# Kernel tuning notes

Measured on AMD Instinct MI355X. Metric: run time of the kernel, lower is better.

Reference implementation:

```python
import jax, jax.numpy as jnp
import numpy as np

OBS_DIM = 128
ACT_DIM = 32
N_AGENTS = 16   # == max_agents; all agents active (obs[...,0]==1)
BATCH = 48
HID = 128       # hid_dim (state encoder output / actor hidden)
QHID = 128      # q_hid_dim (RSA embed dim inside Q)
HEADS = 4       # nn.MultiheadAttention default heads used by Q's RSABlock


def _lin(key, out_d, in_d):
    """torch nn.Linear default init: U(-1/sqrt(fan_in), 1/sqrt(fan_in))."""
    kw, kb = jax.random.split(key)
    s = 1.0 / np.sqrt(in_d)
    w = jax.random.uniform(kw, (out_d, in_d), minval=-s, maxval=s, dtype=jnp.float32)
    b = jax.random.uniform(kb, (out_d,), minval=-s, maxval=s, dtype=jnp.float32)
    return w, b


def linear(x, w, b):
    return x @ w.T + b


def setup_inputs() -> dict:
    key = jax.random.key(0)
    ks = jax.random.split(key, 12)
    obs = jax.random.normal(ks[0], (BATCH, N_AGENTS, OBS_DIM), dtype=jnp.float32)
    obs = obs.at[:, :, 0].set(1.0)  # every agent active
    aw1, ab1 = _lin(ks[1], 2 * HID, OBS_DIM)          # Actor.hidden_layer1
    aw2, ab2 = _lin(ks[2], HID, 2 * HID)              # Actor.hidden_layer2
    aw3, ab3 = _lin(ks[3], ACT_DIM, HID)              # Actor.action_layer
    eow, eob = _lin(ks[4], HID, OBS_DIM)              # StateEncoder.obs_encode_layer
    eaw, eab = _lin(ks[5], HID, OBS_DIM + ACT_DIM)    # StateEncoder.obs_act_encode_layer
    riw, rib = _lin(ks[6], QHID, HID)                 # Q RSABlock.input_layer
    row, rob = _lin(ks[7], QHID, QHID)                # Q RSABlock.output_layer
    miw, mib = _lin(ks[8], 3 * QHID, QHID)            # MHA in_proj
    mow, mob = _lin(ks[9], QHID, QHID)                # MHA out_proj
    qw, qb = _lin(ks[10], 1, QHID)                    # Q.q_layer
    return dict(obs=obs, aw1=aw1, ab1=ab1, aw2=aw2, ab2=ab2, aw3=aw3, ab3=ab3,
                eow=eow, eob=eob, eaw=eaw, eab=eab, riw=riw, rib=rib,
                row=row, rob=rob, miw=miw, mib=mib, mow=mow, mob=mob,
                qw=qw, qb=qb)


def reference(obs, aw1, ab1, aw2, ab2, aw3, ab3, eow, eob, eaw, eab,
              riw, rib, row, rob, miw, mib, mow, mob, qw, qb):
    B, N, _ = obs.shape
    # ---- Actor (all agents active -> fully batched) ----
    x = jax.nn.leaky_relu(linear(obs, aw1, ab1))
    x = jax.nn.leaky_relu(linear(x, aw2, ab2))
    logits = jax.nn.gelu(linear(x, aw3, ab3), approximate=False)  # torch exact GELU
    policy = logits  # (B, N, A)
    # ---- StateEncoder ----
    eo = linear(obs, eow, eob)                                   # (B, N, HID)
    ea = linear(jnp.concatenate([obs, policy], -1), eaw, eab)    # (B, N, HID)
    # counterfactual for agent i: [encoded_obs_i, encoded_obs_act_{j != i}]
    idx = np.array([[j for j in range(N) if j != i] for i in range(N)])  # (N, N-1)
    cf = jnp.concatenate([eo[:, :, None, :], ea[:, idx, :]], axis=2)     # (B, N, N, HID)
    # ---- Q (RSABlock; MHA is batch_first=False -> seq dim = B*N!) ----
    L = B * N
    x1 = jax.nn.relu(linear(cf.reshape(L, N, HID), riw, rib))    # (L, N, E)
    hd = QHID // HEADS
    q, k, v = jnp.split(linear(x1, miw, mib), 3, axis=-1)
    sh = (L, N, HEADS, hd)
    scores = jnp.einsum('lbhd,mbhd->bhlm', q.reshape(sh), k.reshape(sh)) / np.sqrt(hd)
    attn = jax.nn.softmax(scores, axis=-1)                       # (N, H, L, L)
    ao = jnp.einsum('bhlm,mbhd->lbhd', attn, v.reshape(sh)).reshape(L, N, QHID)
    ao = linear(ao, mow, mob)
    ctx = jax.nn.relu(linear(ao + x1, row, rob))                 # (L, N, E)
    qv = linear(ctx, qw, qb).reshape(B, N, N, 1)
    q_values = jnp.sum(qv, axis=2)                               # (B, N, 1)
    policy_flat = policy.reshape(B, N * ACT_DIM)
    return (policy_flat, q_values, eo)
```

## Files before the change

kernel.cpp:

```cpp
#include <hip/hip_runtime.h>
#include <math.h>

static __device__ __forceinline__ float lrelu(float x){ return x > 0.f ? x : 0.01f * x; }

#define OFF_XE    196608
#define OFF_XA    294912
#define OFF_QKVE  393216
#define OFF_QKVA  688128
#define OFF_AOP   983040
#define OFF_DEN   1376256
#define OFF_AOA   1388544
#define OFF_QVE   1572864
#define OFF_QVA   1573632
#define WS_FLOATS 1575072

#define OUT_POL 0
#define OUT_QV  24576
#define OUT_EO  25344

#define SCALE_ATTN 0.17677669529663689f

#define PHASE_FENCE() __builtin_amdgcn_sched_barrier(0)

template<int NCHUNK>
static __device__ __forceinline__ void phase_dot(
    const float* __restrict__ wbase,
    const float* __restrict__ x0, const float* __restrict__ x1,
    const float* __restrict__ x2, const float* __restrict__ x3,
    float* __restrict__ accs)
{
  #pragma unroll 1
  for (int ch = 0; ch < NCHUNK; ++ch) {
    const float4* wp = (const float4*)(wbase + ch * 32);
    float4 wf[8];
    #pragma unroll
    for (int i = 0; i < 8; ++i) wf[i] = wp[i];
    const float* xr0 = x0 + ch * 32;
    const float* xr1 = x1 + ch * 32;
    const float* xr2 = x2 + ch * 32;
    const float* xr3 = x3 + ch * 32;
    #pragma unroll
    for (int r = 0; r < 4; ++r) {
      const float* xr = (r == 0) ? xr0 : (r == 1) ? xr1 : (r == 2) ? xr2 : xr3;
      float ax = 0.f, ay = 0.f, az = 0.f, aw = 0.f;
      #pragma unroll
      for (int i = 0; i < 8; ++i) {
        float4 x = *(const float4*)&xr[i * 4];
        ax = fmaf(x.x, wf[i].x, ax); ay = fmaf(x.y, wf[i].y, ay);
        az = fmaf(x.z, wf[i].z, az); aw = fmaf(x.w, wf[i].w, aw);
      }
      accs[r] += (ax + ay) + (az + aw);
    }
  }
}

static __device__ __forceinline__ void tail_mac2(const float4* __restrict__ wp,
    const float* __restrict__ x0, const float* __restrict__ x1,
    const float* __restrict__ x2, const float* __restrict__ x3,
    float* __restrict__ accs)
{
  float4 wf[2];
  #pragma unroll
  for (int i = 0; i < 2; ++i) wf[i] = wp[i];
  #pragma unroll
  for (int r = 0; r < 4; ++r) {
    const float* xr = (r == 0) ? x0 : (r == 1) ? x1 : (r == 2) ? x2 : x3;
    float ax = 0.f, ay = 0.f, az = 0.f, aw = 0.f;
    #pragma unroll
    for (int i = 0; i < 2; ++i) {
      float4 x = *(const float4*)&xr[i * 4];
      ax = fmaf(x.x, wf[i].x, ax); ay = fmaf(x.y, wf[i].y, ay);
      az = fmaf(x.z, wf[i].z, az); aw = fmaf(x.w, wf[i].w, aw);
    }
    accs[r] += (ax + ay) + (az + aw);
  }
}

__global__ __launch_bounds__(512, 1) void k12ws_front(
    const float* __restrict__ obs,
    const float* __restrict__ aw1, const float* __restrict__ ab1,
    const float* __restrict__ aw2, const float* __restrict__ ab2,
    const float* __restrict__ aw3, const float* __restrict__ ab3,
    const float* __restrict__ eow, const float* __restrict__ eob,
    const float* __restrict__ eaw, const float* __restrict__ eab,
    const float* __restrict__ riw, const float* __restrict__ rib,
    const float* __restrict__ miw, const float* __restrict__ mib,
    float* __restrict__ out, float* __restrict__ ws)
{
  __shared__ float sA[4][256];
  __shared__ float sB[4][160];
  __shared__ float sC[4][128];
  const int t  = threadIdx.x;
  const int bx = blockIdx.x;
  const bool isE = (bx < 192);
  const int r0 = (isE ? bx : bx - 192) * 4;

  const int c = (t & 15) | ((t >> 6) << 4);
  const int h = (t >> 4) & 3;
  const bool h0 = (t & 48) == 0;

  {
    int ri = t >> 7, k = t & 127;
    sB[ri][k] = obs[(r0 + ri) * 128 + k];
  }
  __syncthreads();
  PHASE_FENCE();

  if (isE) {
    {
      float accs[4] = {0.f, 0.f, 0.f, 0.f};
      phase_dot<1>(eow + c * 128 + h * 32,
                   &sB[0][h*32], &sB[1][h*32], &sB[2][h*32], &sB[3][h*32], accs);
      const float bias = eob[c];
      #pragma unroll
      for (int r = 0; r < 4; ++r) {
        float acc = accs[r];
        acc += __shfl_xor(acc, 16);
        acc += __shfl_xor(acc, 32);
        if (h0) {
          float v = acc + bias;
          sA[r][c] = v;
          out[OUT_EO + (r0 + r) * 128 + c] = v;
        }
      }
    }
    __syncthreads();
    PHASE_FENCE();
    {
      float accs[4] = {0.f, 0.f, 0.f, 0.f};
      phase_dot<1>(riw + c * 128 + h * 32,
                   &sA[0][h*32], &sA[1][h*32], &sA[2][h*32], &sA[3][h*32], accs);
      const float bias = rib[c];
      #pragma unroll
      for (int r = 0; r < 4; ++r) {
        float acc = accs[r];
        acc += __shfl_xor(acc, 16);
        acc += __shfl_xor(acc, 32);
        if (h0) {
          float v = fmaxf(acc + bias, 0.f);
          sC[r][c] = v;
          ws[OFF_XE + (r0 + r) * 128 + c] = v;
        }
      }
    }
    __syncthreads();
    PHASE_FENCE();
    #pragma unroll 1
    for (int g = 0; g < 3; ++g) {
      float accs[4] = {0.f, 0.f, 0.f, 0.f};
      phase_dot<1>(miw + (size_t)(g * 128 + c) * 128 + h * 32,
                   &sC[0][h*32], &sC[1][h*32], &sC[2][h*32], &sC[3][h*32], accs);
      const float bias = mib[g * 128 + c];
      #pragma unroll
      for (int r = 0; r < 4; ++r) {
        float acc = accs[r];
        acc += __shfl_xor(acc, 16);
        acc += __shfl_xor(acc, 32);
        if (h0)
          ws[OFF_QKVE + (size_t)(r0 + r) * 384 + g * 128 + c] = acc + bias;
      }
    }
  } else {
    #pragma unroll 1
    for (int g = 0; g < 2; ++g) {
      float accs[4] = {0.f, 0.f, 0.f, 0.f};
      phase_dot<1>(aw1 + (size_t)(g * 128 + c) * 128 + h * 32,
                   &sB[0][h*32], &sB[1][h*32], &sB[2][h*32], &sB[3][h*32], accs);
      const float bias = ab1[g * 128 + c];
      #pragma unroll
      for (int r = 0; r < 4; ++r) {
        float acc = accs[r];
        acc += __shfl_xor(acc, 16);
        acc += __shfl_xor(acc, 32);
        if (h0) sA[r][g * 128 + c] = lrelu(acc + bias);
      }
    }
    __syncthreads();
    PHASE_FENCE();
    {
      float accs[4] = {0.f, 0.f, 0.f, 0.f};
      phase_dot<2>(aw2 + (size_t)c * 256 + h * 64,
                   &sA[0][h*64], &sA[1][h*64], &sA[2][h*64], &sA[3][h*64], accs);
      const float bias = ab2[c];
      #pragma unroll
      for (int r = 0; r < 4; ++r) {
        float acc = accs[r];
        acc += __shfl_xor(acc, 16);
        acc += __shfl_xor(acc, 32);
        if (h0) sC[r][c] = lrelu(acc + bias);
      }
    }
    __syncthreads();
    PHASE_FENCE();
    if (t < 128) {
      const int c2 = (t & 15) | ((t >> 6) << 4);
      const int h2 = (t >> 4) & 3;
      float accs[4] = {0.f, 0.f, 0.f, 0.f};
      phase_dot<1>(aw3 + (size_t)c2 * 128 + h2 * 32,
                   &sC[0][h2*32], &sC[1][h2*32], &sC[2][h2*32], &sC[3][h2*32], accs);
      const float bias = ab3[c2];
      #pragma unroll
      for (int r = 0; r < 4; ++r) {
        float acc = accs[r];
        acc += __shfl_xor(acc, 16);
        acc += __shfl_xor(acc, 32);
        if ((t & 48) == 0) {
          float a = acc + bias;
          float g = 0.5f * a * (1.f + erff(a * 0.70710678118654752f));
          sB[r][128 + c2] = g;
          out[OUT_POL + (r0 + r) * 32 + c2] = g;
        }
      }
    }
    __syncthreads();
    PHASE_FENCE();
    {
      float accs[4] = {0.f, 0.f, 0.f, 0.f};
      const float* wb = eaw + (size_t)c * 160 + h * 40;
      phase_dot<1>(wb, &sB[0][h*40], &sB[1][h*40], &sB[2][h*40], &sB[3][h*40], accs);
      tail_mac2((const float4*)(wb + 32),
                &sB[0][h*40+32], &sB[1][h*40+32], &sB[2][h*40+32], &sB[3][h*40+32], accs);
      const float bias = eab[c];
      #pragma unroll
      for (int r = 0; r < 4; ++r) {
        float acc = accs[r];
        acc += __shfl_xor(acc, 16);
        acc += __shfl_xor(acc, 32);
        if (h0) sA[r][c] = acc + bias;
      }
    }
    __syncthreads();
    PHASE_FENCE();
    {
      float accs[4] = {0.f, 0.f, 0.f, 0.f};
      phase_dot<1>(riw + c * 128 + h * 32,
                   &sA[0][h*32], &sA[1][h*32], &sA[2][h*32], &sA[3][h*32], accs);
      const float bias = rib[c];
      #pragma unroll
      for (int r = 0; r < 4; ++r) {
        float acc = accs[r];
        acc += __shfl_xor(acc, 16);
        acc += __shfl_xor(acc, 32);
        if (h0) {
          float v = fmaxf(acc + bias, 0.f);
          sC[r][c] = v;
          ws[OFF_XA + (r0 + r) * 128 + c] = v;
        }
      }
    }
    __syncthreads();
    PHASE_FENCE();
    #pragma unroll 1
    for (int g = 0; g < 3; ++g) {
      float accs[4] = {0.f, 0.f, 0.f, 0.f};
      phase_dot<1>(miw + (size_t)(g * 128 + c) * 128 + h * 32,
                   &sC[0][h*32], &sC[1][h*32], &sC[2][h*32], &sC[3][h*32], accs);
      const float bias = mib[g * 128 + c];
      #pragma unroll
      for (int r = 0; r < 4; ++r) {
        float acc = accs[r];
        acc += __shfl_xor(acc, 16);
        acc += __shfl_xor(acc, 32);
        if (h0)
          ws[OFF_QKVA + (size_t)(r0 + r) * 384 + g * 128 + c] = acc + bias;
      }
    }
  }
}

__global__ __launch_bounds__(256) void k356_attn(float* __restrict__ ws)
{
  __shared__ __align__(16) union {
    struct { float Qs[16 * 36]; float KsT[32 * 68]; float VsT[32 * 68]; float Ss[16 * 68]; } e;
    struct { float Qb[48 * 33]; float Ka[96 * 33]; float Va[96 * 36]; float Ss[48 * 97]; float rinv[48]; } a;
  } su;
  const int t  = threadIdx.x;
  const int bx = blockIdx.x;

  if (bx < 768) {
    const int l0 = (bx % 48) * 16, h = (bx / 48) & 3, sp = bx / 192;
    const float* qkve = ws + OFF_QKVE;

    for (int f = t; f < 512; f += 256)
      su.e.Qs[(f >> 5) * 36 + (f & 31)] = qkve[(size_t)(l0 + (f >> 5)) * 384 + h * 32 + (f & 31)];
    __syncthreads();

    const int l = t >> 4, j = t & 15, c0 = j * 4;
    float q[32];
    #pragma unroll
    for (int dd = 0; dd < 8; ++dd) {
      float4 qq = *(const float4*)&su.e.Qs[l * 36 + dd * 4];
      q[dd*4+0] = qq.x; q[dd*4+1] = qq.y; q[dd*4+2] = qq.z; q[dd*4+3] = qq.w;
    }
    float o0 = 0.f, o1 = 0.f, dsum = 0.f;

    for (int mt = sp * 3; mt < sp * 3 + 3; ++mt) {
      const int m0 = mt * 64;
      __syncthreads();
      for (int f = t; f < 2048; f += 256) {
        int i = f >> 5, d = f & 31;
        const float* src = qkve + (size_t)(m0 + i) * 384 + h * 32 + d;
        su.e.KsT[d * 68 + i] = src[128];
        su.e.VsT[d * 68 + i] = src[256];
      }
      __syncthreads();

      float s0 = 0.f, s1 = 0.f, s2 = 0.f, s3 = 0.f;
      #pragma unroll
      for (int d = 0; d < 32; ++d) {
        float4 kk = *(const float4*)&su.e.KsT[d * 68 + c0];
        s0 = fmaf(q[d], kk.x, s0); s1 = fmaf(q[d], kk.y, s1);
        s2 = fmaf(q[d], kk.z, s2); s3 = fmaf(q[d], kk.w, s3);
      }
      s0 = expf(s0 * SCALE_ATTN); s1 = expf(s1 * SCALE_ATTN);
      s2 = expf(s2 * SCALE_ATTN); s3 = expf(s3 * SCALE_ATTN);
      float4 sv; sv.x = s0; sv.y = s1; sv.z = s2; sv.w = s3;
      *(float4*)&su.e.Ss[l * 68 + c0] = sv;
      float psum = (s0 + s1) + (s2 + s3);
      psum += __shfl_xor(psum, 1); psum += __shfl_xor(psum, 2);
      psum += __shfl_xor(psum, 4); psum += __shfl_xor(psum, 8);
      dsum += psum;

      float t0x=0.f,t0y=0.f,t0z=0.f,t0w=0.f, t1x=0.f,t1y=0.f,t1z=0.f,t1w=0.f;
      #pragma unroll
      for (int k4 = 0; k4 < 16; ++k4) {
        float4 p  = *(const float4*)&su.e.Ss[l * 68 + k4 * 4];
        float4 va = *(const float4*)&su.e.VsT[j * 68 + k4 * 4];
        float4 vb = *(const float4*)&su.e.VsT[(j + 16) * 68 + k4 * 4];
        t0x = fmaf(p.x, va.x, t0x); t0y = fmaf(p.y, va.y, t0y);
        t0z = fmaf(p.z, va.z, t0z); t0w = fmaf(p.w, va.w, t0w);
        t1x = fmaf(p.x, vb.x, t1x); t1y = fmaf(p.y, vb.y, t1y);
        t1z = fmaf(p.z, vb.z, t1z); t1w = fmaf(p.w, vb.w, t1w);
      }
      o0 += (t0x + t0y) + (t0z + t0w);
      o1 += (t1x + t1y) + (t1z + t1w);
    }

    float* aop = ws + OFF_AOP + (size_t)sp * 98304;
    aop[(size_t)(l0 + l) * 128 + h * 32 + j]      = o0;
    aop[(size_t)(l0 + l) * 128 + h * 32 + j + 16] = o1;
    if (j == 0) ws[OFF_DEN + sp * 3072 + (l0 + l) * 4 + h] = dsum;
  } else {
    const int z  = bx - 768;
    const int j1 = z >> 3;
    const int h  = (z & 7) >> 1, rb = z & 1;
    const int jj = j1 + 1;
    const float* qkva = ws + OFF_QKVA;

    for (int f = t; f < 3072; f += 256) {
      int ml = f >> 5, d = f & 31;
      int bp = ml >> 1, spar = ml & 1;
      int ag = spar ? jj : (jj - 1);
      const float* src = qkva + (size_t)(bp * 16 + ag) * 384 + h * 32 + d;
      su.a.Ka[ml * 33 + d] = src[128];
      su.a.Va[ml * 36 + d] = src[256];
    }
    for (int f = t; f < 1536; f += 256) {
      int ql = f >> 5, d = f & 31;
      int Lb = rb * 48 + ql;
      int b = Lb >> 1, s = Lb & 1;
      int ag = s ? jj : (jj - 1);
      su.a.Qb[ql * 33 + d] = qkva[(size_t)(b * 16 + ag) * 384 + h * 32 + d];
    }
    __syncthreads();

    {
      const int tl = (t >> 4) * 3, tm = (t & 15) * 6;
      float acc[3][6] = {{0.f}};
      #pragma unroll
      for (int d = 0; d < 32; ++d) {
        float qv[3], kv[6];
        #pragma unroll
        for (int r = 0; r < 3; ++r) qv[r] = su.a.Qb[(tl + r) * 33 + d];
        #pragma unroll
        for (int c = 0; c < 6; ++c) kv[c] = su.a.Ka[(tm + c) * 33 + d];
        #pragma unroll
        for (int r = 0; r < 3; ++r)
          #pragma unroll
          for (int c = 0; c < 6; ++c) acc[r][c] = fmaf(qv[r], kv[c], acc[r][c]);
      }
      const float wj = (float)jj, wnj = (float)(16 - jj);
      float rs[3] = {0.f, 0.f, 0.f};
      #pragma unroll
      for (int r = 0; r < 3; ++r)
        #pragma unroll
        for (int c = 0; c < 6; ++c) {
          float w = ((tm + c) & 1) ? wj : wnj;
          float p = w * expf(acc[r][c] * SCALE_ATTN);
          su.a.Ss[(tl + r) * 97 + tm + c] = p;
          rs[r] += p;
        }
      #pragma unroll
      for (int r = 0; r < 3; ++r) {
        rs[r] += __shfl_xor(rs[r], 1); rs[r] += __shfl_xor(rs[r], 2);
        rs[r] += __shfl_xor(rs[r], 4); rs[r] += __shfl_xor(rs[r], 8);
      }
      if ((t & 15) == 0) {
        su.a.rinv[tl + 0] = 1.f / rs[0];
        su.a.rinv[tl + 1] = 1.f / rs[1];
        su.a.rinv[tl + 2] = 1.f / rs[2];
      }
    }
    __syncthreads();

    if (t < 192) {
      const int l0 = (t >> 3) * 2, d0 = (t & 7) * 4;
      float a0x=0.f,a0y=0.f,a0z=0.f,a0w=0.f, a1x=0.f,a1y=0.f,a1z=0.f,a1w=0.f;
      for (int m = 0; m < 96; ++m) {
        float p0 = su.a.Ss[l0 * 97 + m], p1 = su.a.Ss[(l0 + 1) * 97 + m];
        float4 v = *(const float4*)&su.a.Va[m * 36 + d0];
        a0x = fmaf(p0, v.x, a0x); a0y = fmaf(p0, v.y, a0y);
        a0z = fmaf(p0, v.z, a0z); a0w = fmaf(p0, v.w, a0w);
        a1x = fmaf(p1, v.x, a1x); a1y = fmaf(p1, v.y, a1y);
        a1z = fmaf(p1, v.z, a1z); a1w = fmaf(p1, v.w, a1w);
      }
      const float s0 = su.a.rinv[l0], s1 = su.a.rinv[l0 + 1];
      float* ao = ws + OFF_AOA + (size_t)(j1 * 96 + rb * 48 + l0) * 128 + h * 32 + d0;
      float4 o0; o0.x = a0x * s0; o0.y = a0y * s0; o0.z = a0z * s0; o0.w = a0w * s0;
      float4 o1; o1.x = a1x * s1; o1.y = a1y * s1; o1.z = a1z * s1; o1.w = a1w * s1;
      *(float4*)ao = o0;
      *(float4*)(ao + 128) = o1;
    }
  }
}

__global__ __launch_bounds__(512, 1) void k7ab_epi(
    const float* __restrict__ mow, const float* __restrict__ mob,
    const float* __restrict__ roww, const float* __restrict__ robb,
    const float* __restrict__ qw,  const float* __restrict__ qb,
    float* __restrict__ ws)
{
  __shared__ float rows_in[8][132];
  __shared__ float res[8][132];
  __shared__ float t1s[8][132];
  __shared__ float qpart[8][8];
  const int t  = threadIdx.x;
  const int r0 = blockIdx.x * 8;

  for (int s = t; s < 1024; s += 512) {
    int ri = s >> 7, c = s & 127;
    int r = r0 + ri;
    float aoval, x1v;
    if (r < 768) {
      float num = ws[OFF_AOP + 0*98304 + (size_t)r*128 + c]
                + ws[OFF_AOP + 1*98304 + (size_t)r*128 + c]
                + ws[OFF_AOP + 2*98304 + (size_t)r*128 + c]
                + ws[OFF_AOP + 3*98304 + (size_t)r*128 + c];
      int hh = c >> 5;
      float den = ws[OFF_DEN + 0*3072 + r*4 + hh] + ws[OFF_DEN + 1*3072 + r*4 + hh]
                + ws[OFF_DEN + 2*3072 + r*4 + hh] + ws[OFF_DEN + 3*3072 + r*4 + hh];
      aoval = num / den;
      x1v = ws[OFF_XE + r*128 + c];
    } else {
      int rr = r - 768;
      aoval = ws[OFF_AOA + (size_t)rr*128 + c];
      int jx = rr / 96, l96 = rr % 96;
      int b = l96 >> 1, sa = l96 & 1;
      int ag = sa ? (jx + 1) : jx;
      x1v = ws[OFF_XA + (b*16 + ag)*128 + c];
    }
    rows_in[ri][c] = aoval;
    res[ri][c] = x1v;
  }

  const int c = (t & 15) | ((t >> 6) << 4);
  const int h = (t >> 4) & 3;
  const bool h0 = (t & 48) == 0;
  __syncthreads();
  PHASE_FENCE();

  {
    float accs[8] = {0.f,0.f,0.f,0.f,0.f,0.f,0.f,0.f};
    const float4* wp = (const float4*)(mow + c * 128 + h * 32);
    float4 wf[8];
    #pragma unroll
    for (int i = 0; i < 8; ++i) wf[i] = wp[i];
    #pragma unroll
    for (int ri = 0; ri < 8; ++ri) {
      const float* xr = &rows_in[ri][h * 32];
      float ax = 0.f, ay = 0.f, az = 0.f, aw = 0.f;
      #pragma unroll
      for (int i = 0; i < 8; ++i) {
        float4 x = *(const float4*)&xr[i * 4];
        ax = fmaf(x.x, wf[i].x, ax); ay = fmaf(x.y, wf[i].y, ay);
        az = fmaf(x.z, wf[i].z, az); aw = fmaf(x.w, wf[i].w, aw);
      }
      accs[ri] += (ax + ay) + (az + aw);
    }
    const float bias = mob[c];
    #pragma unroll
    for (int ri = 0; ri < 8; ++ri) {
      float acc = accs[ri];
      acc += __shfl_xor(acc, 16);
      acc += __shfl_xor(acc, 32);
      if (h0) t1s[ri][c] = acc + bias + res[ri][c];
    }
  }
  __syncthreads();
  PHASE_FENCE();

  {
    float accs[8] = {0.f,0.f,0.f,0.f,0.f,0.f,0.f,0.f};
    const float4* wp = (const float4*)(roww + c * 128 + h * 32);
    float4 wf[8];
    #pragma unroll
    for (int i = 0; i < 8; ++i) wf[i] = wp[i];
    #pragma unroll
    for (int ri = 0; ri < 8; ++ri) {
      const float* xr = &t1s[ri][h * 32];
      float ax = 0.f, ay = 0.f, az = 0.f, aw = 0.f;
      #pragma unroll
      for (int i = 0; i < 8; ++i) {
        float4 x = *(const float4*)&xr[i * 4];
        ax = fmaf(x.x, wf[i].x, ax); ay = fmaf(x.y, wf[i].y, ay);
        az = fmaf(x.z, wf[i].z, az); aw = fmaf(x.w, wf[i].w, aw);
      }
      accs[ri] += (ax + ay) + (az + aw);
    }
    const float bias = robb[c];
    const float qwc  = qw[c];
    #pragma unroll
    for (int ri = 0; ri < 8; ++ri) {
      float acc = accs[ri];
      acc += __shfl_xor(acc, 16);
      acc += __shfl_xor(acc, 32);
      float ctx = fmaxf(acc + bias, 0.f);
      float p = h0 ? qwc * ctx : 0.f;
      p += __shfl_xor(p, 1);  p += __shfl_xor(p, 2);  p += __shfl_xor(p, 4);
      p += __shfl_xor(p, 8);  p += __shfl_xor(p, 16); p += __shfl_xor(p, 32);
      if ((t & 63) == 0) qpart[ri][t >> 6] = p;
    }
  }
  __syncthreads();

  if (t < 8) {
    float qv = ((qpart[t][0] + qpart[t][1]) + (qpart[t][2] + qpart[t][3]))
             + ((qpart[t][4] + qpart[t][5]) + (qpart[t][6] + qpart[t][7])) + qb[0];
    int r = r0 + t;
    if (r < 768) ws[OFF_QVE + r] = qv;
    else         ws[OFF_QVA + (r - 768)] = qv;
  }
}

__global__ __launch_bounds__(256) void k8_final(const float* __restrict__ ws, float* __restrict__ out)
{
  const int idx = blockIdx.x * 256 + threadIdx.x;
  if (idx >= 768) return;
  const int b = idx >> 4, i = idx & 15;
  float acc = ws[OFF_QVE + idx];
  const float* qva = ws + OFF_QVA;
  #pragma unroll
  for (int j = 1; j <= 15; ++j) {
    int s = (i >= j) ? 0 : 1;
    acc += qva[(j - 1) * 96 + b * 2 + s];
  }
  out[OUT_QV + idx] = acc;
}

extern "C" void kernel_launch(void* const* d_in, const int* in_sizes, int n_in,
                              void* d_out, int out_size, void* d_ws, size_t ws_size,
                              hipStream_t stream)
{
  (void)in_sizes; (void)n_in; (void)out_size;
  if (ws_size < (size_t)WS_FLOATS * 4) return;

  const float* obs = (const float*)d_in[0];
  const float* aw1 = (const float*)d_in[1];
  const float* ab1 = (const float*)d_in[2];
  const float* aw2 = (const float*)d_in[3];
  const float* ab2 = (const float*)d_in[4];
  const float* aw3 = (const float*)d_in[5];
  const float* ab3 = (const float*)d_in[6];
  const float* eow = (const float*)d_in[7];
  const float* eob = (const float*)d_in[8];
  const float* eaw = (const float*)d_in[9];
  const float* eab = (const float*)d_in[10];
  const float* riw = (const float*)d_in[11];
  const float* rib = (const float*)d_in[12];
  const float* roww= (const float*)d_in[13];
  const float* robb= (const float*)d_in[14];
  const float* miw = (const float*)d_in[15];
  const float* mib = (const float*)d_in[16];
  const float* mow = (const float*)d_in[17];
  const float* mob = (const float*)d_in[18];
  const float* qw  = (const float*)d_in[19];
  const float* qb  = (const float*)d_in[20];

  float* out = (float*)d_out;
  float* ws  = (float*)d_ws;

  k12ws_front<<<dim3(384), dim3(512), 0, stream>>>(obs, aw1, ab1, aw2, ab2, aw3, ab3,
                                                   eow, eob, eaw, eab, riw, rib, miw, mib,
                                                   out, ws);
  k356_attn<<<dim3(888), dim3(256), 0, stream>>>(ws);
  k7ab_epi<<<dim3(276), dim3(512), 0, stream>>>(mow, mob, roww, robb, qw, qb, ws);
  k8_final<<<dim3(3), dim3(256), 0, stream>>>(ws, out);
}
```

Before: 184.7 us.

## Rotate K-chunk order per split, interleave front blocks, halve epilogue block size

In the front kernel each K-split group now reads its weight and shared-memory chunks in a rotated order, with the rotation set by the split index. The intent is to spread LDS bank and cache accesses across the four splits. Encoder and actor blocks are now interleaved by block index rather than placed in two contiguous halves, which should balance the two work types across CUs. The epilogue kernel moves from 512 to 256 threads with a 2-way K split over two chunks each, which cuts shuffle reductions and allows more blocks per CU, at the cost of more serial work per thread.

```diff
diff --git a/kernel.cpp b/kernel.cpp
--- a/kernel.cpp
+++ b/kernel.cpp
@@ -27,14 +27,14 @@
     const float* __restrict__ wbase,
     const float* __restrict__ x0, const float* __restrict__ x1,
     const float* __restrict__ x2, const float* __restrict__ x3,
-    float* __restrict__ accs)
+    float* __restrict__ accs, int rot)
 {
   #pragma unroll 1
   for (int ch = 0; ch < NCHUNK; ++ch) {
     const float4* wp = (const float4*)(wbase + ch * 32);
     float4 wf[8];
     #pragma unroll
-    for (int i = 0; i < 8; ++i) wf[i] = wp[i];
+    for (int s = 0; s < 8; ++s) wf[s] = wp[(s + rot) & 7];
     const float* xr0 = x0 + ch * 32;
     const float* xr1 = x1 + ch * 32;
     const float* xr2 = x2 + ch * 32;
@@ -44,10 +44,10 @@
       const float* xr = (r == 0) ? xr0 : (r == 1) ? xr1 : (r == 2) ? xr2 : xr3;
       float ax = 0.f, ay = 0.f, az = 0.f, aw = 0.f;
       #pragma unroll
-      for (int i = 0; i < 8; ++i) {
-        float4 x = *(const float4*)&xr[i * 4];
-        ax = fmaf(x.x, wf[i].x, ax); ay = fmaf(x.y, wf[i].y, ay);
-        az = fmaf(x.z, wf[i].z, az); aw = fmaf(x.w, wf[i].w, aw);
+      for (int s = 0; s < 8; ++s) {
+        float4 x = *(const float4*)&xr[((s + rot) & 7) * 4];
+        ax = fmaf(x.x, wf[s].x, ax); ay = fmaf(x.y, wf[s].y, ay);
+        az = fmaf(x.z, wf[s].z, az); aw = fmaf(x.w, wf[s].w, aw);
       }
       accs[r] += (ax + ay) + (az + aw);
     }
@@ -92,8 +92,8 @@
   __shared__ float sC[4][128];
   const int t  = threadIdx.x;
   const int bx = blockIdx.x;
-  const bool isE = (bx < 192);
-  const int r0 = (isE ? bx : bx - 192) * 4;
+  const bool isE = (bx & 1) == 0;
+  const int r0 = (bx >> 1) * 4;
 
   const int c = (t & 15) | ((t >> 6) << 4);
   const int h = (t >> 4) & 3;
@@ -110,7 +110,7 @@
     {
       float accs[4] = {0.f, 0.f, 0.f, 0.f};
       phase_dot<1>(eow + c * 128 + h * 32,
-                   &sB[0][h*32], &sB[1][h*32], &sB[2][h*32], &sB[3][h*32], accs);
+                   &sB[0][h*32], &sB[1][h*32], &sB[2][h*32], &sB[3][h*32], accs, h);
       const float bias = eob[c];
       #pragma unroll
       for (int r = 0; r < 4; ++r) {
@@ -129,7 +129,7 @@
     {
       float accs[4] = {0.f, 0.f, 0.f, 0.f};
       phase_dot<1>(riw + c * 128 + h * 32,
-                   &sA[0][h*32], &sA[1][h*32], &sA[2][h*32], &sA[3][h*32], accs);
+                   &sA[0][h*32], &sA[1][h*32], &sA[2][h*32], &sA[3][h*32], accs, h);
       const float bias = rib[c];
       #pragma unroll
       for (int r = 0; r < 4; ++r) {
@@ -149,7 +149,7 @@
     for (int g = 0; g < 3; ++g) {
       float accs[4] = {0.f, 0.f, 0.f, 0.f};
       phase_dot<1>(miw + (size_t)(g * 128 + c) * 128 + h * 32,
-                   &sC[0][h*32], &sC[1][h*32], &sC[2][h*32], &sC[3][h*32], accs);
+                   &sC[0][h*32], &sC[1][h*32], &sC[2][h*32], &sC[3][h*32], accs, h);
       const float bias = mib[g * 128 + c];
       #pragma unroll
       for (int r = 0; r < 4; ++r) {
@@ -165,7 +165,7 @@
     for (int g = 0; g < 2; ++g) {
       float accs[4] = {0.f, 0.f, 0.f, 0.f};
       phase_dot<1>(aw1 + (size_t)(g * 128 + c) * 128 + h * 32,
-                   &sB[0][h*32], &sB[1][h*32], &sB[2][h*32], &sB[3][h*32], accs);
+                   &sB[0][h*32], &sB[1][h*32], &sB[2][h*32], &sB[3][h*32], accs, h);
       const float bias = ab1[g * 128 + c];
       #pragma unroll
       for (int r = 0; r < 4; ++r) {
@@ -180,7 +180,7 @@
     {
       float accs[4] = {0.f, 0.f, 0.f, 0.f};
       phase_dot<2>(aw2 + (size_t)c * 256 + h * 64,
-                   &sA[0][h*64], &sA[1][h*64], &sA[2][h*64], &sA[3][h*64], accs);
+                   &sA[0][h*64], &sA[1][h*64], &sA[2][h*64], &sA[3][h*64], accs, h);
       const float bias = ab2[c];
       #pragma unroll
       for (int r = 0; r < 4; ++r) {
@@ -197,7 +197,7 @@
       const int h2 = (t >> 4) & 3;
       float accs[4] = {0.f, 0.f, 0.f, 0.f};
       phase_dot<1>(aw3 + (size_t)c2 * 128 + h2 * 32,
-                   &sC[0][h2*32], &sC[1][h2*32], &sC[2][h2*32], &sC[3][h2*32], accs);
+                   &sC[0][h2*32], &sC[1][h2*32], &sC[2][h2*32], &sC[3][h2*32], accs, h2);
       const float bias = ab3[c2];
       #pragma unroll
       for (int r = 0; r < 4; ++r) {
@@ -217,7 +217,7 @@
     {
       float accs[4] = {0.f, 0.f, 0.f, 0.f};
       const float* wb = eaw + (size_t)c * 160 + h * 40;
-      phase_dot<1>(wb, &sB[0][h*40], &sB[1][h*40], &sB[2][h*40], &sB[3][h*40], accs);
+      phase_dot<1>(wb, &sB[0][h*40], &sB[1][h*40], &sB[2][h*40], &sB[3][h*40], accs, 0);
       tail_mac2((const float4*)(wb + 32),
                 &sB[0][h*40+32], &sB[1][h*40+32], &sB[2][h*40+32], &sB[3][h*40+32], accs);
       const float bias = eab[c];
@@ -234,7 +234,7 @@
     {
       float accs[4] = {0.f, 0.f, 0.f, 0.f};
       phase_dot<1>(riw + c * 128 + h * 32,
-                   &sA[0][h*32], &sA[1][h*32], &sA[2][h*32], &sA[3][h*32], accs);
+                   &sA[0][h*32], &sA[1][h*32], &sA[2][h*32], &sA[3][h*32], accs, h);
       const float bias = rib[c];
       #pragma unroll
       for (int r = 0; r < 4; ++r) {
@@ -254,7 +254,7 @@
     for (int g = 0; g < 3; ++g) {
       float accs[4] = {0.f, 0.f, 0.f, 0.f};
       phase_dot<1>(miw + (size_t)(g * 128 + c) * 128 + h * 32,
-                   &sC[0][h*32], &sC[1][h*32], &sC[2][h*32], &sC[3][h*32], accs);
+                   &sC[0][h*32], &sC[1][h*32], &sC[2][h*32], &sC[3][h*32], accs, h);
       const float bias = mib[g * 128 + c];
       #pragma unroll
       for (int r = 0; r < 4; ++r) {
@@ -424,7 +424,7 @@
   }
 }
 
-__global__ __launch_bounds__(512, 1) void k7ab_epi(
+__global__ __launch_bounds__(256) void k7ab_epi(
     const float* __restrict__ mow, const float* __restrict__ mob,
     const float* __restrict__ roww, const float* __restrict__ robb,
     const float* __restrict__ qw,  const float* __restrict__ qb,
@@ -433,11 +433,11 @@
   __shared__ float rows_in[8][132];
   __shared__ float res[8][132];
   __shared__ float t1s[8][132];
-  __shared__ float qpart[8][8];
+  __shared__ float qpart[8][4];
   const int t  = threadIdx.x;
   const int r0 = blockIdx.x * 8;
 
-  for (int s = t; s < 1024; s += 512) {
+  for (int s = t; s < 1024; s += 256) {
     int ri = s >> 7, c = s & 127;
     int r = r0 + ri;
     float aoval, x1v;
@@ -463,69 +463,72 @@
     res[ri][c] = x1v;
   }
 
-  const int c = (t & 15) | ((t >> 6) << 4);
-  const int h = (t >> 4) & 3;
-  const bool h0 = (t & 48) == 0;
+  const int c = (t & 31) | ((t >> 6) << 5);
+  const int h = (t >> 5) & 1;
   __syncthreads();
-  PHASE_FENCE();
 
   {
     float accs[8] = {0.f,0.f,0.f,0.f,0.f,0.f,0.f,0.f};
-    const float4* wp = (const float4*)(mow + c * 128 + h * 32);
-    float4 wf[8];
-    #pragma unroll
-    for (int i = 0; i < 8; ++i) wf[i] = wp[i];
-    #pragma unroll
-    for (int ri = 0; ri < 8; ++ri) {
-      const float* xr = &rows_in[ri][h * 32];
-      float ax = 0.f, ay = 0.f, az = 0.f, aw = 0.f;
-      #pragma unroll
-      for (int i = 0; i < 8; ++i) {
-        float4 x = *(const float4*)&xr[i * 4];
-        ax = fmaf(x.x, wf[i].x, ax); ay = fmaf(x.y, wf[i].y, ay);
-        az = fmaf(x.z, wf[i].z, az); aw = fmaf(x.w, wf[i].w, aw);
-      }
-      accs[ri] += (ax + ay) + (az + aw);
+    const float* wb = mow + c * 128 + h * 64;
+    #pragma unroll 1
+    for (int ch = 0; ch < 2; ++ch) {
+      const float4* wp = (const float4*)(wb + ch * 32);
+      float4 wf[8];
+      #pragma unroll
+      for (int i = 0; i < 8; ++i) wf[i] = wp[i];
+      #pragma unroll
+      for (int ri = 0; ri < 8; ++ri) {
+        const float* xr = &rows_in[ri][h * 64 + ch * 32];
+        float ax = 0.f, ay = 0.f, az = 0.f, aw = 0.f;
+        #pragma unroll
+        for (int i = 0; i < 8; ++i) {
+          float4 x = *(const float4*)&xr[i * 4];
+          ax = fmaf(x.x, wf[i].x, ax); ay = fmaf(x.y, wf[i].y, ay);
+          az = fmaf(x.z, wf[i].z, az); aw = fmaf(x.w, wf[i].w, aw);
+        }
+        accs[ri] += (ax + ay) + (az + aw);
+      }
     }
     const float bias = mob[c];
     #pragma unroll
     for (int ri = 0; ri < 8; ++ri) {
       float acc = accs[ri];
-      acc += __shfl_xor(acc, 16);
       acc += __shfl_xor(acc, 32);
-      if (h0) t1s[ri][c] = acc + bias + res[ri][c];
+      if (h == 0) t1s[ri][c] = acc + bias + res[ri][c];
     }
   }
   __syncthreads();
-  PHASE_FENCE();
 
   {
     float accs[8] = {0.f,0.f,0.f,0.f,0.f,0.f,0.f,0.f};
-    const float4* wp = (const float4*)(roww + c * 128 + h * 32);
-    float4 wf[8];
-    #pragma unroll
-    for (int i = 0; i < 8; ++i) wf[i] = wp[i];
-    #pragma unroll
-    for (int ri = 0; ri < 8; ++ri) {
-      const float* xr = &t1s[ri][h * 32];
-      float ax = 0.f, ay = 0.f, az = 0.f, aw = 0.f;
-      #pragma unroll
-      for (int i = 0; i < 8; ++i) {
-        float4 x = *(const float4*)&xr[i * 4];
-        ax = fmaf(x.x, wf[i].x, ax); ay = fmaf(x.y, wf[i].y, ay);
-        az = fmaf(x.z, wf[i].z, az); aw = fmaf(x.w, wf[i].w, aw);
-      }
-      accs[ri] += (ax + ay) + (az + aw);
+    const float* wb = roww + c * 128 + h * 64;
+    #pragma unroll 1
+    for (int ch = 0; ch < 2; ++ch) {
+      const float4* wp = (const float4*)(wb + ch * 32);
+      float4 wf[8];
+      #pragma unroll
+      for (int i = 0; i < 8; ++i) wf[i] = wp[i];
+      #pragma unroll
+      for (int ri = 0; ri < 8; ++ri) {
+        const float* xr = &t1s[ri][h * 64 + ch * 32];
+        float ax = 0.f, ay = 0.f, az = 0.f, aw = 0.f;
+        #pragma unroll
+        for (int i = 0; i < 8; ++i) {
+          float4 x = *(const float4*)&xr[i * 4];
+          ax = fmaf(x.x, wf[i].x, ax); ay = fmaf(x.y, wf[i].y, ay);
+          az = fmaf(x.z, wf[i].z, az); aw = fmaf(x.w, wf[i].w, aw);
+        }
+        accs[ri] += (ax + ay) + (az + aw);
+      }
     }
     const float bias = robb[c];
     const float qwc  = qw[c];
     #pragma unroll
     for (int ri = 0; ri < 8; ++ri) {
       float acc = accs[ri];
-      acc += __shfl_xor(acc, 16);
       acc += __shfl_xor(acc, 32);
       float ctx = fmaxf(acc + bias, 0.f);
-      float p = h0 ? qwc * ctx : 0.f;
+      float p = (h == 0) ? qwc * ctx : 0.f;
       p += __shfl_xor(p, 1);  p += __shfl_xor(p, 2);  p += __shfl_xor(p, 4);
       p += __shfl_xor(p, 8);  p += __shfl_xor(p, 16); p += __shfl_xor(p, 32);
       if ((t & 63) == 0) qpart[ri][t >> 6] = p;
@@ -534,8 +537,7 @@
   __syncthreads();
 
   if (t < 8) {
-    float qv = ((qpart[t][0] + qpart[t][1]) + (qpart[t][2] + qpart[t][3]))
-             + ((qpart[t][4] + qpart[t][5]) + (qpart[t][6] + qpart[t][7])) + qb[0];
+    float qv = (qpart[t][0] + qpart[t][1]) + (qpart[t][2] + qpart[t][3]) + qb[0];
     int r = r0 + t;
     if (r < 768) ws[OFF_QVE + r] = qv;
     else         ws[OFF_QVA + (r - 768)] = qv;
@@ -593,6 +595,6 @@
                                                    eow, eob, eaw, eab, riw, rib, miw, mib,
                                                    out, ws);
   k356_attn<<<dim3(888), dim3(256), 0, stream>>>(ws);
-  k7ab_epi<<<dim3(276), dim3(512), 0, stream>>>(mow, mob, roww, robb, qw, qb, ws);
+  k7ab_epi<<<dim3(276), dim3(256), 0, stream>>>(mow, mob, roww, robb, qw, qb, ws);
   k8_final<<<dim3(3), dim3(256), 0, stream>>>(ws, out);
 }
```

Result: no change. 185.0 us (+0.2%).
